# Performance work log

Hardware: AMD Instinct MI355X
Metric: run time of the kernel (lower is better)

Reference implementation:

```python
import jax, jax.numpy as jnp
import numpy as np

DIM = 512
HEADS = 8
WINDOW = 128


def setup_inputs() -> dict:
    key = jax.random.key(0)
    k1, k2, k3, k4 = jax.random.split(key, 4)
    x = jax.random.normal(k1, (16, 4096, DIM), dtype=jnp.float32)
    w_qkv = jax.random.normal(k2, (3 * DIM, DIM), dtype=jnp.float32) * 0.02
    w_proj = jax.random.normal(k3, (DIM, DIM), dtype=jnp.float32) * 0.02
    b_proj = jax.random.normal(k4, (DIM,), dtype=jnp.float32) * 0.02
    return {"x": x, "w_qkv": w_qkv, "w_proj": w_proj, "b_proj": b_proj}


def reference(x, w_qkv, w_proj, b_proj):
    B0, T0, C = x.shape
    H = HEADS
    hd = C // H
    scale = hd ** (-0.5)
    W = WINDOW
    # split into independent windows: [B*T/W, W, C]
    xw = x.reshape(-1, W, C)
    Bw = xw.shape[0]
    # qkv projection (no bias), reshape to [3, Bw, H, W, hd]
    qkv = (xw @ w_qkv.T).reshape(Bw, W, 3, H, hd).transpose(2, 0, 3, 1, 4)
    q, k, v = qkv[0], qkv[1], qkv[2]
    # scaled scores per window: [Bw, H, W, W]
    attn = jnp.einsum("bhqd,bhkd->bhqk", q, k) * scale
    causal_mask = jnp.tril(jnp.ones((W, W), dtype=bool))
    attn = jnp.where(causal_mask, attn, -jnp.inf)
    attn = jax.nn.softmax(attn, axis=-1)
    out = jnp.einsum("bhqk,bhkd->bhqd", attn, v)  # [Bw, H, W, hd]
    out = out.transpose(0, 2, 1, 3).reshape(Bw, W, C)
    out = out @ w_proj.T + b_proj
    return out.reshape(B0, T0, C)
```

## Files before the change

kernel.cpp:

```cpp
#include <hip/hip_runtime.h>
#include <stdint.h>


typedef unsigned short ushort_t;
typedef __attribute__((ext_vector_type(8))) short short8;
typedef __attribute__((ext_vector_type(4))) float f32x4;
typedef __attribute__((ext_vector_type(4))) float f4v;
typedef __attribute__((ext_vector_type(4))) unsigned short us4;

static __device__ __forceinline__ unsigned short f2bf(float f) {
  unsigned int u = __float_as_uint(f);
  u += 0x7FFFu + ((u >> 16) & 1u);
  return (unsigned short)(u >> 16);
}

static __device__ __forceinline__ void gl_lds16(const ushort_t* g, ushort_t* l) {
  __builtin_amdgcn_global_load_lds(
      (const __attribute__((address_space(1))) void*)g,
      (__attribute__((address_space(3))) void*)l, 16, 0, 0);
}

__global__ __launch_bounds__(256) void cast_f32_bf16(const float* __restrict__ in,
                                                     ushort_t* __restrict__ out, int n4) {
  int i = blockIdx.x * 256 + threadIdx.x;
  if (i >= n4) return;
  f4v v = ((const f4v*)in)[i];
  us4 o;
  o.x = f2bf(v.x); o.y = f2bf(v.y); o.z = f2bf(v.z); o.w = f2bf(v.w);
  ((us4*)out)[i] = o;
}

__global__ __launch_bounds__(256) void qkv_gemm(const ushort_t* __restrict__ A,
                                                const ushort_t* __restrict__ B,
                                                ushort_t* __restrict__ qk,
                                                ushort_t* __restrict__ vT) {
  __shared__ __align__(16) ushort_t As[128 * 64];
  __shared__ __align__(16) ushort_t Bs[128 * 64];
  const int tid = threadIdx.x;
  const int lane = tid & 63;
  const int wv = tid >> 6;
  const int wr = wv >> 1, wc = wv & 1;
  const int m0 = blockIdx.y << 7;
  const int n0 = blockIdx.x << 7;
  const int lr = lane & 15;
  const int lg = lane >> 4;
  const int sw = lr & 7;

  f32x4 acc[4][4] = {};

  const int grow = tid >> 3;
  const int gcol = (((tid & 7) ^ (grow & 7)) << 3);
  const ushort_t* gA = A + (size_t)(m0 + grow) * 512 + gcol;
  const ushort_t* gB = B + (size_t)(n0 + grow) * 512 + gcol;

  for (int kk = 0; kk < 512; kk += 64) {
#pragma unroll
    for (int r = 0; r < 4; ++r) {
      gl_lds16(gA + (size_t)(r * 32) * 512 + kk, As + (size_t)(r * 256 + wv * 64) * 8);
      gl_lds16(gB + (size_t)(r * 32) * 512 + kk, Bs + (size_t)(r * 256 + wv * 64) * 8);
    }
    __syncthreads();
#pragma unroll
    for (int ks = 0; ks < 2; ++ks) {
      const int co = ((((ks << 2) | lg) ^ sw) << 3);
      short8 a[4], b[4];
#pragma unroll
      for (int mi = 0; mi < 4; ++mi)
        a[mi] = *(const short8*)(As + (wr * 64 + mi * 16 + lr) * 64 + co);
#pragma unroll
      for (int ni = 0; ni < 4; ++ni)
        b[ni] = *(const short8*)(Bs + (wc * 64 + ni * 16 + lr) * 64 + co);
#pragma unroll
      for (int mi = 0; mi < 4; ++mi)
#pragma unroll
        for (int ni = 0; ni < 4; ++ni)
          acc[mi][ni] = __builtin_amdgcn_mfma_f32_16x16x32_bf16(a[mi], b[ni], acc[mi][ni], 0, 0, 0);
    }
    __syncthreads();
  }

  const int lg4 = lg << 2;
  if (n0 < 1024) {
#pragma unroll
    for (int mi = 0; mi < 4; ++mi) {
      const int rbase = m0 + wr * 64 + mi * 16 + lg4;
#pragma unroll
      for (int ni = 0; ni < 4; ++ni) {
        const int col = n0 + wc * 64 + ni * 16 + lr;
#pragma unroll
        for (int rg = 0; rg < 4; ++rg)
          qk[(size_t)(rbase + rg) * 1024 + col] = f2bf(acc[mi][ni][rg]);
      }
    }
  } else {
    const int win = blockIdx.y;
#pragma unroll
    for (int mi = 0; mi < 4; ++mi) {
      const int t0 = wr * 64 + mi * 16 + lg4;
#pragma unroll
      for (int ni = 0; ni < 4; ++ni) {
        const int c = n0 - 1024 + wc * 64 + ni * 16 + lr;
        const int h = c >> 6, d = c & 63;
        us4 o;
        o.x = f2bf(acc[mi][ni][0]); o.y = f2bf(acc[mi][ni][1]);
        o.z = f2bf(acc[mi][ni][2]); o.w = f2bf(acc[mi][ni][3]);
        *(us4*)(vT + (size_t)((win * 8 + h) * 64 + d) * 128 + t0) = o;
      }
    }
  }
}

__global__ __launch_bounds__(256) void attn_kernel(const ushort_t* __restrict__ qk,
                                                   const ushort_t* __restrict__ vT,
                                                   ushort_t* __restrict__ attn_out) {
  __shared__ __align__(16) ushort_t smem[25856];
  ushort_t* qs = smem;
  ushort_t* ks_ = smem + 8704;
  ushort_t* vs = smem + 17408;
  ushort_t* ps = smem;

  const int tid = threadIdx.x;
  const int lane = tid & 63;
  const int wv = tid >> 6;
  const int win = blockIdx.x >> 3;
  const int h = blockIdx.x & 7;
  const int lr = lane & 15;
  const int lg = lane >> 4;
  const int lk = lg << 3;
  const int lg4 = lg << 2;

  const size_t qbase = (size_t)win * 128 * 1024 + h * 64;
#pragma unroll
  for (int r = 0; r < 4; ++r) {
    const int c = r * 256 + tid;
    const int t = c >> 3, d8 = (c & 7) << 3;
    short8 vq = *(const short8*)(qk + qbase + (size_t)t * 1024 + d8);
    short8 vk = *(const short8*)(qk + qbase + 512 + (size_t)t * 1024 + d8);
    *(short8*)(qs + t * 68 + d8) = vq;
    *(short8*)(ks_ + t * 68 + d8) = vk;
  }
  const size_t vbase = (size_t)(win * 8 + h) * 64 * 128;
#pragma unroll
  for (int r = 0; r < 4; ++r) {
    const int c = r * 256 + tid;
    const int d = c >> 4, t8 = (c & 15) << 3;
    short8 vvv = *(const short8*)(vT + vbase + (size_t)d * 128 + t8);
    *(short8*)(vs + d * 132 + t8) = vvv;
  }
  __syncthreads();

  const int rt[2] = {wv, 7 - wv};

  f32x4 sacc[2][8] = {};
#pragma unroll
  for (int ks2 = 0; ks2 < 2; ++ks2) {
    const int kb = ks2 * 32 + lk;
    short8 a0 = *(const short8*)(qs + (rt[0] * 16 + lr) * 68 + kb);
    short8 a1 = *(const short8*)(qs + (rt[1] * 16 + lr) * 68 + kb);
#pragma unroll
    for (int ni = 0; ni < 8; ++ni) {
      if (ni <= rt[1]) {
        short8 b = *(const short8*)(ks_ + (ni * 16 + lr) * 68 + kb);
        if (ni <= rt[0])
          sacc[0][ni] = __builtin_amdgcn_mfma_f32_16x16x32_bf16(a0, b, sacc[0][ni], 0, 0, 0);
        sacc[1][ni] = __builtin_amdgcn_mfma_f32_16x16x32_bf16(a1, b, sacc[1][ni], 0, 0, 0);
      }
    }
  }

  const float scale = 0.125f;
  float rs[2][4];
#pragma unroll
  for (int mi = 0; mi < 2; ++mi) {
    const int rb = rt[mi] * 16;
#pragma unroll
    for (int rg = 0; rg < 4; ++rg) {
      const int row = rb + lg4 + rg;
      float m = -1e30f;
#pragma unroll
      for (int ni = 0; ni < 8; ++ni) {
        if (ni <= rt[mi]) {
          const int col = ni * 16 + lr;
          float v = sacc[mi][ni][rg] * scale;
          v = (col <= row) ? v : -1e30f;
          sacc[mi][ni][rg] = v;
          m = fmaxf(m, v);
        }
      }
      m = fmaxf(m, __shfl_xor(m, 1));
      m = fmaxf(m, __shfl_xor(m, 2));
      m = fmaxf(m, __shfl_xor(m, 4));
      m = fmaxf(m, __shfl_xor(m, 8));
      float s = 0.f;
#pragma unroll
      for (int ni = 0; ni < 8; ++ni) {
        if (ni <= rt[mi]) {
          float p = __expf(sacc[mi][ni][rg] - m);
          sacc[mi][ni][rg] = p;
          s += p;
        }
      }
      s += __shfl_xor(s, 1);
      s += __shfl_xor(s, 2);
      s += __shfl_xor(s, 4);
      s += __shfl_xor(s, 8);
      rs[mi][rg] = 1.0f / s;
    }
  }

  __syncthreads();

#pragma unroll
  for (int mi = 0; mi < 2; ++mi) {
    const int r = rt[mi];
    const int rb = r * 16;
#pragma unroll
    for (int ni = 0; ni < 8; ++ni) {
      if (ni <= r) {
#pragma unroll
        for (int rg = 0; rg < 4; ++rg)
          ps[(rb + lg4 + rg) * 132 + ni * 16 + lr] = f2bf(sacc[mi][ni][rg]);
      }
    }
    if (!(r & 1)) {
#pragma unroll
      for (int rg = 0; rg < 4; ++rg)
        ps[(rb + lg4 + rg) * 132 + (r + 1) * 16 + lr] = 0;
    }
  }

  f32x4 oacc[2][4] = {};
#pragma unroll
  for (int ks2 = 0; ks2 < 4; ++ks2) {
    const int kb = ks2 * 32 + lk;
    if (ks2 <= (rt[1] >> 1)) {
      short8 a1 = *(const short8*)(ps + (rt[1] * 16 + lr) * 132 + kb);
#pragma unroll
      for (int nd = 0; nd < 4; ++nd) {
        short8 b = *(const short8*)(vs + (nd * 16 + lr) * 132 + kb);
        oacc[1][nd] = __builtin_amdgcn_mfma_f32_16x16x32_bf16(a1, b, oacc[1][nd], 0, 0, 0);
      }
      if (ks2 <= (rt[0] >> 1)) {
        short8 a0 = *(const short8*)(ps + (rt[0] * 16 + lr) * 132 + kb);
#pragma unroll
        for (int nd = 0; nd < 4; ++nd) {
          short8 b = *(const short8*)(vs + (nd * 16 + lr) * 132 + kb);
          oacc[0][nd] = __builtin_amdgcn_mfma_f32_16x16x32_bf16(a0, b, oacc[0][nd], 0, 0, 0);
        }
      }
    }
  }

  const size_t obase = (size_t)win * 128 * 512 + h * 64;
#pragma unroll
  for (int mi = 0; mi < 2; ++mi) {
    const int rb = rt[mi] * 16;
#pragma unroll
    for (int nd = 0; nd < 4; ++nd)
#pragma unroll
      for (int rg = 0; rg < 4; ++rg) {
        const int row = rb + lg4 + rg;
        const int col = nd * 16 + lr;
        attn_out[obase + (size_t)row * 512 + col] = f2bf(oacc[mi][nd][rg] * rs[mi][rg]);
      }
  }
}

__global__ __launch_bounds__(256) void proj_gemm(const ushort_t* __restrict__ A,
                                                 const ushort_t* __restrict__ B,
                                                 const float* __restrict__ bias,
                                                 float* __restrict__ out) {
  __shared__ __align__(16) ushort_t As[128 * 64];
  __shared__ __align__(16) ushort_t Bs[128 * 64];
  const int tid = threadIdx.x;
  const int lane = tid & 63;
  const int wv = tid >> 6;
  const int wr = wv >> 1, wc = wv & 1;
  const int m0 = blockIdx.y << 7;
  const int n0 = blockIdx.x << 7;
  const int lr = lane & 15;
  const int lg = lane >> 4;
  const int sw = lr & 7;

  f32x4 acc[4][4] = {};

  const int grow = tid >> 3;
  const int gcol = (((tid & 7) ^ (grow & 7)) << 3);
  const ushort_t* gA = A + (size_t)(m0 + grow) * 512 + gcol;
  const ushort_t* gB = B + (size_t)(n0 + grow) * 512 + gcol;

  for (int kk = 0; kk < 512; kk += 64) {
#pragma unroll
    for (int r = 0; r < 4; ++r) {
      gl_lds16(gA + (size_t)(r * 32) * 512 + kk, As + (size_t)(r * 256 + wv * 64) * 8);
      gl_lds16(gB + (size_t)(r * 32) * 512 + kk, Bs + (size_t)(r * 256 + wv * 64) * 8);
    }
    __syncthreads();
#pragma unroll
    for (int ks = 0; ks < 2; ++ks) {
      const int co = ((((ks << 2) | lg) ^ sw) << 3);
      short8 a[4], b[4];
#pragma unroll
      for (int mi = 0; mi < 4; ++mi)
        a[mi] = *(const short8*)(As + (wr * 64 + mi * 16 + lr) * 64 + co);
#pragma unroll
      for (int ni = 0; ni < 4; ++ni)
        b[ni] = *(const short8*)(Bs + (wc * 64 + ni * 16 + lr) * 64 + co);
#pragma unroll
      for (int mi = 0; mi < 4; ++mi)
#pragma unroll
        for (int ni = 0; ni < 4; ++ni)
          acc[mi][ni] = __builtin_amdgcn_mfma_f32_16x16x32_bf16(a[mi], b[ni], acc[mi][ni], 0, 0, 0);
    }
    __syncthreads();
  }

  const int lg4 = lg << 2;
#pragma unroll
  for (int mi = 0; mi < 4; ++mi) {
    const int rbase = m0 + wr * 64 + mi * 16 + lg4;
#pragma unroll
    for (int ni = 0; ni < 4; ++ni) {
      const int col = n0 + wc * 64 + ni * 16 + lr;
      const float bv = bias[col];
#pragma unroll
      for (int rg = 0; rg < 4; ++rg)
        out[(size_t)(rbase + rg) * 512 + col] = acc[mi][ni][rg] + bv;
    }
  }
}

extern "C" void kernel_launch(void* const* d_in, const int* in_sizes, int n_in,
                              void* d_out, int out_size, void* d_ws, size_t ws_size,
                              hipStream_t stream) {
  const float* x      = (const float*)d_in[0];
  const float* w_qkv  = (const float*)d_in[1];
  const float* w_proj = (const float*)d_in[2];
  const float* b_proj = (const float*)d_in[3];
  float* out = (float*)d_out;

  char* ws = (char*)d_ws;
  ushort_t* x_bf     = (ushort_t*)(ws);
  ushort_t* qk_ws    = (ushort_t*)(ws + 67108864);
  ushort_t* vT_ws    = (ushort_t*)(ws + 67108864 + 134217728);
  ushort_t* attn_ws  = (ushort_t*)(ws + 67108864 + 134217728 + 67108864);
  ushort_t* wqkv_bf  = (ushort_t*)(ws + 335544320);
  ushort_t* wproj_bf = (ushort_t*)(ws + 337117184);

  cast_f32_bf16<<<32768, 256, 0, stream>>>(x, x_bf, 8388608);
  cast_f32_bf16<<<768, 256, 0, stream>>>(w_qkv, wqkv_bf, 196608);
  cast_f32_bf16<<<256, 256, 0, stream>>>(w_proj, wproj_bf, 65536);

  qkv_gemm<<<dim3(12, 512), 256, 0, stream>>>(x_bf, wqkv_bf, qk_ws, vT_ws);
  attn_kernel<<<4096, 256, 0, stream>>>(qk_ws, vT_ws, attn_ws);
  proj_gemm<<<dim3(4, 512), 256, 0, stream>>>(attn_ws, wproj_bf, b_proj, out);
}
```

Before: 550.9 us.

## Swizzle attention LDS, drop softmax max pass, MFMA row sums, swap GEMM grid order

Attention tiles in shared memory now use an XOR swizzle instead of row padding, which shrinks LDS use and aims to avoid bank conflicts. Softmax skips the row-max subtraction and shuffle reductions: it applies exp2 with the scale folded in and gets row sums from an extra MFMA against a ones vector. The GEMM launch grids are transposed so adjacent blocks iterate over M, which changes L2 reuse of the weight tiles. Dropping the max subtraction risks overflow if scores become large.

```diff
diff --git a/kernel.cpp b/kernel.cpp
--- a/kernel.cpp
+++ b/kernel.cpp
@@ -40,8 +40,8 @@
   const int lane = tid & 63;
   const int wv = tid >> 6;
   const int wr = wv >> 1, wc = wv & 1;
-  const int m0 = blockIdx.y << 7;
-  const int n0 = blockIdx.x << 7;
+  const int m0 = blockIdx.x << 7;
+  const int n0 = blockIdx.y << 7;
   const int lr = lane & 15;
   const int lg = lane >> 4;
   const int sw = lr & 7;
@@ -93,7 +93,7 @@
       }
     }
   } else {
-    const int win = blockIdx.y;
+    const int win = blockIdx.x;
 #pragma unroll
     for (int mi = 0; mi < 4; ++mi) {
       const int t0 = wr * 64 + mi * 16 + lg4;
@@ -113,10 +113,10 @@
 __global__ __launch_bounds__(256) void attn_kernel(const ushort_t* __restrict__ qk,
                                                    const ushort_t* __restrict__ vT,
                                                    ushort_t* __restrict__ attn_out) {
-  __shared__ __align__(16) ushort_t smem[25856];
+  __shared__ __align__(16) ushort_t smem[24576];
   ushort_t* qs = smem;
-  ushort_t* ks_ = smem + 8704;
-  ushort_t* vs = smem + 17408;
+  ushort_t* ks_ = smem + 8192;
+  ushort_t* vs = smem + 16384;
   ushort_t* ps = smem;
 
   const int tid = threadIdx.x;
@@ -126,26 +126,27 @@
   const int h = blockIdx.x & 7;
   const int lr = lane & 15;
   const int lg = lane >> 4;
-  const int lk = lg << 3;
   const int lg4 = lg << 2;
+  const int sw = lr & 7;
 
   const size_t qbase = (size_t)win * 128 * 1024 + h * 64;
 #pragma unroll
   for (int r = 0; r < 4; ++r) {
-    const int c = r * 256 + tid;
-    const int t = c >> 3, d8 = (c & 7) << 3;
-    short8 vq = *(const short8*)(qk + qbase + (size_t)t * 1024 + d8);
-    short8 vk = *(const short8*)(qk + qbase + 512 + (size_t)t * 1024 + d8);
-    *(short8*)(qs + t * 68 + d8) = vq;
-    *(short8*)(ks_ + t * 68 + d8) = vk;
+    const int g = r * 256 + tid;
+    const int t = g >> 3, ch = g & 7;
+    short8 vq = *(const short8*)(qk + qbase + (size_t)t * 1024 + ch * 8);
+    short8 vk = *(const short8*)(qk + qbase + 512 + (size_t)t * 1024 + ch * 8);
+    const int st = t * 64 + ((ch ^ (t & 7)) << 3);
+    *(short8*)(qs + st) = vq;
+    *(short8*)(ks_ + st) = vk;
   }
   const size_t vbase = (size_t)(win * 8 + h) * 64 * 128;
 #pragma unroll
   for (int r = 0; r < 4; ++r) {
-    const int c = r * 256 + tid;
-    const int d = c >> 4, t8 = (c & 15) << 3;
-    short8 vvv = *(const short8*)(vT + vbase + (size_t)d * 128 + t8);
-    *(short8*)(vs + d * 132 + t8) = vvv;
+    const int g = r * 256 + tid;
+    const int d = g >> 4, ch = g & 15;
+    short8 vvv = *(const short8*)(vT + vbase + (size_t)d * 128 + ch * 8);
+    *(short8*)(vs + d * 128 + ((ch ^ (d & 7)) << 3)) = vvv;
   }
   __syncthreads();
 
@@ -154,13 +155,13 @@
   f32x4 sacc[2][8] = {};
 #pragma unroll
   for (int ks2 = 0; ks2 < 2; ++ks2) {
-    const int kb = ks2 * 32 + lk;
-    short8 a0 = *(const short8*)(qs + (rt[0] * 16 + lr) * 68 + kb);
-    short8 a1 = *(const short8*)(qs + (rt[1] * 16 + lr) * 68 + kb);
+    const int co = ((((ks2 << 2) | lg) ^ sw) << 3);
+    short8 a0 = *(const short8*)(qs + (rt[0] * 16 + lr) * 64 + co);
+    short8 a1 = *(const short8*)(qs + (rt[1] * 16 + lr) * 64 + co);
 #pragma unroll
     for (int ni = 0; ni < 8; ++ni) {
       if (ni <= rt[1]) {
-        short8 b = *(const short8*)(ks_ + (ni * 16 + lr) * 68 + kb);
+        short8 b = *(const short8*)(ks_ + (ni * 16 + lr) * 64 + co);
         if (ni <= rt[0])
           sacc[0][ni] = __builtin_amdgcn_mfma_f32_16x16x32_bf16(a0, b, sacc[0][ni], 0, 0, 0);
         sacc[1][ni] = __builtin_amdgcn_mfma_f32_16x16x32_bf16(a1, b, sacc[1][ni], 0, 0, 0);
@@ -168,48 +169,9 @@
     }
   }
 
-  const float scale = 0.125f;
-  float rs[2][4];
-#pragma unroll
-  for (int mi = 0; mi < 2; ++mi) {
-    const int rb = rt[mi] * 16;
-#pragma unroll
-    for (int rg = 0; rg < 4; ++rg) {
-      const int row = rb + lg4 + rg;
-      float m = -1e30f;
-#pragma unroll
-      for (int ni = 0; ni < 8; ++ni) {
-        if (ni <= rt[mi]) {
-          const int col = ni * 16 + lr;
-          float v = sacc[mi][ni][rg] * scale;
-          v = (col <= row) ? v : -1e30f;
-          sacc[mi][ni][rg] = v;
-          m = fmaxf(m, v);
-        }
-      }
-      m = fmaxf(m, __shfl_xor(m, 1));
-      m = fmaxf(m, __shfl_xor(m, 2));
-      m = fmaxf(m, __shfl_xor(m, 4));
-      m = fmaxf(m, __shfl_xor(m, 8));
-      float s = 0.f;
-#pragma unroll
-      for (int ni = 0; ni < 8; ++ni) {
-        if (ni <= rt[mi]) {
-          float p = __expf(sacc[mi][ni][rg] - m);
-          sacc[mi][ni][rg] = p;
-          s += p;
-        }
-      }
-      s += __shfl_xor(s, 1);
-      s += __shfl_xor(s, 2);
-      s += __shfl_xor(s, 4);
-      s += __shfl_xor(s, 8);
-      rs[mi][rg] = 1.0f / s;
-    }
-  }
-
   __syncthreads();
 
+  const float C = 0.125f * 1.44269504f;
 #pragma unroll
   for (int mi = 0; mi < 2; ++mi) {
     const int r = rt[mi];
@@ -218,50 +180,71 @@
     for (int ni = 0; ni < 8; ++ni) {
       if (ni <= r) {
 #pragma unroll
-        for (int rg = 0; rg < 4; ++rg)
-          ps[(rb + lg4 + rg) * 132 + ni * 16 + lr] = f2bf(sacc[mi][ni][rg]);
+        for (int rg = 0; rg < 4; ++rg) {
+          const int row = rb + lg4 + rg;
+          const int col = ni * 16 + lr;
+          float e = __builtin_exp2f(sacc[mi][ni][rg] * C);
+          e = (col <= row) ? e : 0.0f;
+          ps[row * 128 + ((((col >> 3) ^ (row & 7)) << 3) | (col & 7))] = f2bf(e);
+        }
       }
     }
     if (!(r & 1)) {
-#pragma unroll
-      for (int rg = 0; rg < 4; ++rg)
-        ps[(rb + lg4 + rg) * 132 + (r + 1) * 16 + lr] = 0;
-    }
-  }
+      const int col = (r + 1) * 16 + lr;
+#pragma unroll
+      for (int rg = 0; rg < 4; ++rg) {
+        const int row = rb + lg4 + rg;
+        ps[row * 128 + ((((col >> 3) ^ (row & 7)) << 3) | (col & 7))] = 0;
+      }
+    }
+  }
+
+  const short one_bf = (short)0x3F80;
+  short8 ones;
+#pragma unroll
+  for (int j = 0; j < 8; ++j) ones[j] = (lr == 0) ? one_bf : (short)0;
 
   f32x4 oacc[2][4] = {};
+  f32x4 sm[2] = {};
 #pragma unroll
   for (int ks2 = 0; ks2 < 4; ++ks2) {
-    const int kb = ks2 * 32 + lk;
+    const int co = ((((ks2 << 2) | lg) ^ sw) << 3);
     if (ks2 <= (rt[1] >> 1)) {
-      short8 a1 = *(const short8*)(ps + (rt[1] * 16 + lr) * 132 + kb);
-#pragma unroll
-      for (int nd = 0; nd < 4; ++nd) {
-        short8 b = *(const short8*)(vs + (nd * 16 + lr) * 132 + kb);
-        oacc[1][nd] = __builtin_amdgcn_mfma_f32_16x16x32_bf16(a1, b, oacc[1][nd], 0, 0, 0);
-      }
+      short8 b[4];
+#pragma unroll
+      for (int nd = 0; nd < 4; ++nd)
+        b[nd] = *(const short8*)(vs + (nd * 16 + lr) * 128 + co);
+      short8 a1 = *(const short8*)(ps + (rt[1] * 16 + lr) * 128 + co);
+#pragma unroll
+      for (int nd = 0; nd < 4; ++nd)
+        oacc[1][nd] = __builtin_amdgcn_mfma_f32_16x16x32_bf16(a1, b[nd], oacc[1][nd], 0, 0, 0);
+      sm[1] = __builtin_amdgcn_mfma_f32_16x16x32_bf16(a1, ones, sm[1], 0, 0, 0);
       if (ks2 <= (rt[0] >> 1)) {
-        short8 a0 = *(const short8*)(ps + (rt[0] * 16 + lr) * 132 + kb);
-#pragma unroll
-        for (int nd = 0; nd < 4; ++nd) {
-          short8 b = *(const short8*)(vs + (nd * 16 + lr) * 132 + kb);
-          oacc[0][nd] = __builtin_amdgcn_mfma_f32_16x16x32_bf16(a0, b, oacc[0][nd], 0, 0, 0);
-        }
-      }
-    }
-  }
-
+        short8 a0 = *(const short8*)(ps + (rt[0] * 16 + lr) * 128 + co);
+#pragma unroll
+        for (int nd = 0; nd < 4; ++nd)
+          oacc[0][nd] = __builtin_amdgcn_mfma_f32_16x16x32_bf16(a0, b[nd], oacc[0][nd], 0, 0, 0);
+        sm[0] = __builtin_amdgcn_mfma_f32_16x16x32_bf16(a0, ones, sm[0], 0, 0, 0);
+      }
+    }
+  }
+
+  const int src = lane & 48;
   const size_t obase = (size_t)win * 128 * 512 + h * 64;
 #pragma unroll
   for (int mi = 0; mi < 2; ++mi) {
     const int rb = rt[mi] * 16;
+    float rsv[4];
+#pragma unroll
+    for (int rg = 0; rg < 4; ++rg)
+      rsv[rg] = 1.0f / __shfl(sm[mi][rg], src);
 #pragma unroll
     for (int nd = 0; nd < 4; ++nd)
 #pragma unroll
       for (int rg = 0; rg < 4; ++rg) {
         const int row = rb + lg4 + rg;
         const int col = nd * 16 + lr;
-        attn_out[obase + (size_t)row * 512 + col] = f2bf(oacc[mi][nd][rg] * rs[mi][rg]);
+        attn_out[obase + (size_t)row * 512 + col] = f2bf(oacc[mi][nd][rg] * rsv[rg]);
       }
   }
 }
@@ -276,8 +259,8 @@
   const int lane = tid & 63;
   const int wv = tid >> 6;
   const int wr = wv >> 1, wc = wv & 1;
-  const int m0 = blockIdx.y << 7;
-  const int n0 = blockIdx.x << 7;
+  const int m0 = blockIdx.x << 7;
+  const int n0 = blockIdx.y << 7;
   const int lr = lane & 15;
   const int lg = lane >> 4;
   const int sw = lr & 7;
@@ -351,7 +334,7 @@
   cast_f32_bf16<<<768, 256, 0, stream>>>(w_qkv, wqkv_bf, 196608);
   cast_f32_bf16<<<256, 256, 0, stream>>>(w_proj, wproj_bf, 65536);
 
-  qkv_gemm<<<dim3(12, 512), 256, 0, stream>>>(x_bf, wqkv_bf, qk_ws, vT_ws);
+  qkv_gemm<<<dim3(512, 12), 256, 0, stream>>>(x_bf, wqkv_bf, qk_ws, vT_ws);
   attn_kernel<<<4096, 256, 0, stream>>>(qk_ws, vT_ws, attn_ws);
-  proj_gemm<<<dim3(4, 512), 256, 0, stream>>>(attn_ws, wproj_bf, b_proj, out);
-}
+  proj_gemm<<<dim3(512, 4), 256, 0, stream>>>(attn_ws, wproj_bf, b_proj, out);
+}
```

After: 518.8 us. -5.8%, faster.
